# Kernel optimization log

Hardware: AMD Instinct MI355X
Metric: run time of the kernel (lower is better)

## Reference

```python
import jax, jax.numpy as jnp
import numpy as np

EPS_NORM = 1e-05
EPS_LOG = 1e-10


def _rmsnorm(x, scale, eps=EPS_NORM):
    var = jnp.mean(jnp.square(x), axis=-1, keepdims=True)
    return x * jax.lax.rsqrt(var + eps) * scale


def setup_inputs() -> dict:
    key = jax.random.key(0)
    k1, k2, k3, k4 = jax.random.split(key, 4)
    B, S, H, E, V = 1, 256, 2560, 10, 50257
    hidden_states = jax.random.normal(k1, (B, S, H), dtype=jnp.float32)
    embedding_matrix = jax.random.normal(k2, (V, H), dtype=jnp.float32) * 0.02
    norm_scale = jnp.ones((H,), dtype=jnp.float32)
    expert_weights = jax.random.normal(k3, (E, H, H), dtype=jnp.float32) * 0.02
    gate_weight = jax.random.normal(k4, (H, E), dtype=jnp.float32) * 0.02
    return {
        "hidden_states": hidden_states,
        "embedding_matrix": embedding_matrix,
        "norm_scale": norm_scale,
        "expert_weights": expert_weights,
        "gate_weight": gate_weight,
    }


def reference(hidden_states, embedding_matrix, norm_scale, expert_weights, gate_weight):
    # RMSNorm
    h = _rmsnorm(hidden_states, norm_scale)  # (B,S,H)
    # Per-expert dense transforms (no bias): (B,S,E,H)
    expert_hidden = jnp.einsum("bsh,ehd->bsed", h, expert_weights)
    # Shared-embedding projection: (B,S,E,V)
    expert_logits = jnp.einsum("bsed,vd->bsev", expert_hidden, embedding_matrix)
    # temperature == 1.0, no scaling
    expert_probs = jax.nn.softmax(expert_logits.astype(jnp.float32), axis=-1)
    # Gate over experts
    gate_logits = jnp.einsum("bsh,he->bse", h, gate_weight)
    gate_weights = jax.nn.softmax(gate_logits, axis=-1)  # (B,S,E)
    # Mixture of softmaxes, then log
    mixed_probs = jnp.einsum("bse,bsev->bsv", gate_weights, expert_probs)
    logits = jnp.log(mixed_probs + EPS_LOG)
    return logits
```

## Files before the change

### kernel.cpp

```cpp
#include <hip/hip_runtime.h>
#include <hip/hip_bf16.h>

#define SEQ   256
#define HDIM  2560
#define NEXP  10
#define VOC   50257
#define VP    50304
#define M2    2560
#define KTILES (HDIM/32)

#define O_H      0
#define O_EH     1310720
#define O_GATE   14417920
#define O_STATS  14428160
#define O_LOG    14448640
#define O_EMB    272005120
#define EMB_BYTES 257315840
#define WS_NEED  (O_EMB + (size_t)EMB_BYTES)

typedef __attribute__((ext_vector_type(8))) short bf16x8;
typedef __attribute__((ext_vector_type(4))) float f32x4;

union BPack { bf16x8 v; __hip_bfloat162 h[4]; };

__device__ __forceinline__ void ld_lds16(const void* g, void* l) {
  __builtin_amdgcn_global_load_lds(
      (const __attribute__((address_space(1))) void*)g,
      (__attribute__((address_space(3))) void*)l, 16, 0, 0);
}

__global__ __launch_bounds__(256) void cvt_emb_kernel(
    const float* __restrict__ src, __hip_bfloat16* __restrict__ dst) {
  const size_t n8 = (size_t)VOC * HDIM / 8;
  size_t i = (size_t)blockIdx.x * 256 + threadIdx.x;
  const size_t stride = (size_t)gridDim.x * 256;
  const f32x4* s4 = (const f32x4*)src;
  bf16x8* d8 = (bf16x8*)dst;
  for (; i < n8; i += stride) {
    const f32x4 x0 = s4[2 * i];
    const f32x4 x1 = s4[2 * i + 1];
    BPack u;
    u.h[0] = __float22bfloat162_rn(make_float2(x0.x, x0.y));
    u.h[1] = __float22bfloat162_rn(make_float2(x0.z, x0.w));
    u.h[2] = __float22bfloat162_rn(make_float2(x1.x, x1.y));
    u.h[3] = __float22bfloat162_rn(make_float2(x1.z, x1.w));
    d8[i] = u.v;
  }
}

__global__ __launch_bounds__(256) void rmsnorm_gate_kernel(
    const float* __restrict__ x, const float* __restrict__ scale,
    const float* __restrict__ gw, __hip_bfloat16* __restrict__ hbf,
    float* __restrict__ gate) {
  const int s   = blockIdx.x;
  const int tid = threadIdx.x;
  const int lane = tid & 63, wave = tid >> 6;
  const float* xr = x + (size_t)s * HDIM;

  float xi[10];
  float ss = 0.f;
#pragma unroll
  for (int j = 0; j < 10; ++j) {
    xi[j] = xr[j * 256 + tid];
    ss += xi[j] * xi[j];
  }
#pragma unroll
  for (int off = 32; off >= 1; off >>= 1) ss += __shfl_down(ss, off);
  __shared__ float red[4];
  if (lane == 0) red[wave] = ss;
  __syncthreads();
  const float tot = red[0] + red[1] + red[2] + red[3];
  const float inv = rsqrtf(tot / (float)HDIM + 1e-5f);

  float ge[NEXP];
#pragma unroll
  for (int e = 0; e < NEXP; ++e) ge[e] = 0.f;
#pragma unroll
  for (int j = 0; j < 10; ++j) {
    const int i = j * 256 + tid;
    const float hv = xi[j] * inv * scale[i];
    hbf[(size_t)s * HDIM + i] = __float2bfloat16(hv);
#pragma unroll
    for (int e = 0; e < NEXP; ++e) ge[e] += hv * gw[i * NEXP + e];
  }
#pragma unroll
  for (int e = 0; e < NEXP; ++e) {
#pragma unroll
    for (int off = 32; off >= 1; off >>= 1) ge[e] += __shfl_down(ge[e], off);
  }
  __shared__ float gred[4][NEXP];
  if (lane == 0) {
#pragma unroll
    for (int e = 0; e < NEXP; ++e) gred[wave][e] = ge[e];
  }
  __syncthreads();
  if (tid == 0) {
    float g[NEXP], mx = -1e30f, sum = 0.f;
#pragma unroll
    for (int e = 0; e < NEXP; ++e) {
      g[e] = gred[0][e] + gred[1][e] + gred[2][e] + gred[3][e];
      mx = fmaxf(mx, g[e]);
    }
#pragma unroll
    for (int e = 0; e < NEXP; ++e) { g[e] = __expf(g[e] - mx); sum += g[e]; }
#pragma unroll
    for (int e = 0; e < NEXP; ++e) gate[s * NEXP + e] = g[e] / sum;
  }
}

__global__ __launch_bounds__(256) void gemm1_kernel(
    const __hip_bfloat16* __restrict__ A, const float* __restrict__ W,
    __hip_bfloat16* __restrict__ EH) {
  __shared__ short As[128 * 32];
  __shared__ float Bs[32 * 128];

  const int tid = threadIdx.x;
  const int bm = blockIdx.x, bn = blockIdx.y, e = blockIdx.z;
  const int wave = tid >> 6, lane = tid & 63;
  const int wr = (wave & 1) * 64, wc = (wave >> 1) * 64;
  const int lm = lane & 15, lq = lane >> 4;
  const int row0 = bm * 128, col0 = bn * 128;
  const float* We = W + (size_t)e * HDIM * HDIM;

  f32x4 acc[4][4];
#pragma unroll
  for (int i = 0; i < 4; ++i)
#pragma unroll
    for (int j = 0; j < 4; ++j) acc[i][j] = (f32x4){0.f, 0.f, 0.f, 0.f};

  for (int kt = 0; kt < KTILES; ++kt) {
    const int k0 = kt * 32;
#pragma unroll
    for (int c = 0; c < 2; ++c) {
      const int ar = c * 64 + (tid >> 2);
      ld_lds16(A + (size_t)(row0 + ar) * HDIM + k0 + (tid & 3) * 8,
               (char*)As + c * 4096 + tid * 16);
    }
#pragma unroll
    for (int c = 0; c < 4; ++c) {
      const int L = c * 256 + tid;
      const int brow = L >> 5;
      const int cg = (L & 31) ^ (((brow >> 3) & 1) << 2);
      ld_lds16(We + (size_t)(k0 + brow) * HDIM + col0 + cg * 4,
               (char*)Bs + c * 4096 + tid * 16);
    }
    __syncthreads();

    bf16x8 a[4];
#pragma unroll
    for (int mt = 0; mt < 4; ++mt)
      a[mt] = *(const bf16x8*)&As[(wr + mt * 16 + lm) * 32 + lq * 8];
#pragma unroll
    for (int nt = 0; nt < 4; ++nt) {
      const int n = wc + nt * 16 + lm;
      const int slot = (n >> 2) ^ ((lq & 1) << 2);
      const int base = slot * 4 + (n & 3);
      BPack u;
#pragma unroll
      for (int jj = 0; jj < 4; ++jj) {
        const float f0 = Bs[(lq * 8 + 2 * jj) * 128 + base];
        const float f1 = Bs[(lq * 8 + 2 * jj + 1) * 128 + base];
        u.h[jj] = __float22bfloat162_rn(make_float2(f0, f1));
      }
#pragma unroll
      for (int mt = 0; mt < 4; ++mt)
        acc[mt][nt] = __builtin_amdgcn_mfma_f32_16x16x32_bf16(
            a[mt], u.v, acc[mt][nt], 0, 0, 0);
    }
    __syncthreads();
  }

#pragma unroll
  for (int mt = 0; mt < 4; ++mt) {
#pragma unroll
    for (int nt = 0; nt < 4; ++nt) {
#pragma unroll
      for (int i = 0; i < 4; ++i) {
        const int r = row0 + wr + mt * 16 + lq * 4 + i;
        const int d = col0 + wc + nt * 16 + lm;
        EH[((size_t)e * SEQ + r) * HDIM + d] = __float2bfloat16(acc[mt][nt][i]);
      }
    }
  }
}

__global__ __launch_bounds__(256) void gemm2_bf16_kernel(
    const __hip_bfloat16* __restrict__ A, const __hip_bfloat16* __restrict__ B,
    __hip_bfloat16* __restrict__ Cl) {
  __shared__ short As[128 * 32];
  __shared__ short Bs[128 * 32];

  const int tid = threadIdx.x;
  const int orig = blockIdx.x;
  const int q = 7860 / 8, rr = 7860 % 8;
  const int xcd = orig & 7, idx = orig >> 3;
  const int wg = (xcd < rr ? xcd * (q + 1) : rr * (q + 1) + (xcd - rr) * q) + idx;
  const int bm = wg % 20, bn = wg / 20;

  const int wave = tid >> 6, lane = tid & 63;
  const int wr = (wave & 1) * 64, wc = (wave >> 1) * 64;
  const int lm = lane & 15, lq = lane >> 4;
  const int row0 = bm * 128, col0 = bn * 128;

  f32x4 acc[4][4];
#pragma unroll
  for (int i = 0; i < 4; ++i)
#pragma unroll
    for (int j = 0; j < 4; ++j) acc[i][j] = (f32x4){0.f, 0.f, 0.f, 0.f};

  for (int kt = 0; kt < KTILES; ++kt) {
    const int k0 = kt * 32;
#pragma unroll
    for (int c = 0; c < 2; ++c) {
      const int ar = c * 64 + (tid >> 2);
      ld_lds16(A + (size_t)(row0 + ar) * HDIM + k0 + (tid & 3) * 8,
               (char*)As + c * 4096 + tid * 16);
    }
#pragma unroll
    for (int c = 0; c < 2; ++c) {
      const int br = c * 64 + (tid >> 2);
      const int vr = min(col0 + br, VOC - 1);
      ld_lds16(B + (size_t)vr * HDIM + k0 + (tid & 3) * 8,
               (char*)Bs + c * 4096 + tid * 16);
    }
    __syncthreads();

    bf16x8 a[4], b[4];
#pragma unroll
    for (int mt = 0; mt < 4; ++mt)
      a[mt] = *(const bf16x8*)&As[(wr + mt * 16 + lm) * 32 + lq * 8];
#pragma unroll
    for (int nt = 0; nt < 4; ++nt)
      b[nt] = *(const bf16x8*)&Bs[(wc + nt * 16 + lm) * 32 + lq * 8];
#pragma unroll
    for (int nt = 0; nt < 4; ++nt)
#pragma unroll
      for (int mt = 0; mt < 4; ++mt)
        acc[mt][nt] = __builtin_amdgcn_mfma_f32_16x16x32_bf16(
            a[mt], b[nt], acc[mt][nt], 0, 0, 0);
    __syncthreads();
  }

#pragma unroll
  for (int mt = 0; mt < 4; ++mt) {
#pragma unroll
    for (int nt = 0; nt < 4; ++nt) {
#pragma unroll
      for (int i = 0; i < 4; ++i) {
        const int r = row0 + wr + mt * 16 + lq * 4 + i;
        const int v = col0 + wc + nt * 16 + lm;
        const float val = (v < VOC) ? acc[mt][nt][i] : -INFINITY;
        Cl[(size_t)r * VP + v] = __float2bfloat16(val);
      }
    }
  }
}

__global__ __launch_bounds__(256) void gemm2_kernel(
    const __hip_bfloat16* __restrict__ A, const float* __restrict__ B,
    __hip_bfloat16* __restrict__ Cl) {
  __shared__ short As[128 * 32];
  __shared__ float Bs[128 * 32];

  const int tid = threadIdx.x;
  const int bm = blockIdx.x, bn = blockIdx.y;
  const int wave = tid >> 6, lane = tid & 63;
  const int wr = (wave & 1) * 64, wc = (wave >> 1) * 64;
  const int lm = lane & 15, lq = lane >> 4;
  const int row0 = bm * 128, col0 = bn * 128;

  f32x4 acc[4][4];
#pragma unroll
  for (int i = 0; i < 4; ++i)
#pragma unroll
    for (int j = 0; j < 4; ++j) acc[i][j] = (f32x4){0.f, 0.f, 0.f, 0.f};

  for (int kt = 0; kt < KTILES; ++kt) {
    const int k0 = kt * 32;
#pragma unroll
    for (int c = 0; c < 2; ++c) {
      const int ar = c * 64 + (tid >> 2);
      ld_lds16(A + (size_t)(row0 + ar) * HDIM + k0 + (tid & 3) * 8,
               (char*)As + c * 4096 + tid * 16);
    }
#pragma unroll
    for (int c = 0; c < 4; ++c) {
      const int L = c * 256 + tid;
      const int brow = L >> 3;
      const int cg = (L & 7) ^ (brow & 7);
      const int vr = min(col0 + brow, VOC - 1);
      ld_lds16(B + (size_t)vr * HDIM + k0 + cg * 4,
               (char*)Bs + c * 4096 + tid * 16);
    }
    __syncthreads();

    bf16x8 a[4];
#pragma unroll
    for (int mt = 0; mt < 4; ++mt)
      a[mt] = *(const bf16x8*)&As[(wr + mt * 16 + lm) * 32 + lq * 8];
#pragma unroll
    for (int nt = 0; nt < 4; ++nt) {
      const int n = wc + nt * 16 + lm;
      const int r7 = n & 7;
      const f32x4 b0 = *(const f32x4*)&Bs[n * 32 + (((2 * lq) ^ r7) << 2)];
      const f32x4 b1 = *(const f32x4*)&Bs[n * 32 + (((2 * lq + 1) ^ r7) << 2)];
      BPack u;
      u.h[0] = __float22bfloat162_rn(make_float2(b0.x, b0.y));
      u.h[1] = __float22bfloat162_rn(make_float2(b0.z, b0.w));
      u.h[2] = __float22bfloat162_rn(make_float2(b1.x, b1.y));
      u.h[3] = __float22bfloat162_rn(make_float2(b1.z, b1.w));
#pragma unroll
      for (int mt = 0; mt < 4; ++mt)
        acc[mt][nt] = __builtin_amdgcn_mfma_f32_16x16x32_bf16(
            a[mt], u.v, acc[mt][nt], 0, 0, 0);
    }
    __syncthreads();
  }

#pragma unroll
  for (int mt = 0; mt < 4; ++mt) {
#pragma unroll
    for (int nt = 0; nt < 4; ++nt) {
#pragma unroll
      for (int i = 0; i < 4; ++i) {
        const int r = row0 + wr + mt * 16 + lq * 4 + i;
        const int v = col0 + wc + nt * 16 + lm;
        const float val = (v < VOC) ? acc[mt][nt][i] : -INFINITY;
        Cl[(size_t)r * VP + v] = __float2bfloat16(val);
      }
    }
  }
}

__global__ __launch_bounds__(256) void softmax_stats_kernel(
    const __hip_bfloat16* __restrict__ Cl, const float* __restrict__ gate,
    float* __restrict__ stats) {
  const int r = blockIdx.x;
  const int tid = threadIdx.x;
  const bf16x8* row = (const bf16x8*)(Cl + (size_t)r * VP);

  float m = -1e30f, l = 0.f;
  for (int c = tid; c < VP / 8; c += 256) {
    const bf16x8 ch = row[c];
    float x[8];
#pragma unroll
    for (int j = 0; j < 8; ++j)
      x[j] = __bfloat162float(((const __hip_bfloat16*)&ch)[j]);
    float lm = x[0];
#pragma unroll
    for (int j = 1; j < 8; ++j) lm = fmaxf(lm, x[j]);
    if (lm > m) { l *= __expf(m - lm); m = lm; }
#pragma unroll
    for (int j = 0; j < 8; ++j) l += __expf(x[j] - m);
  }
#pragma unroll
  for (int off = 32; off >= 1; off >>= 1) {
    const float m2 = __shfl_down(m, off);
    const float l2 = __shfl_down(l, off);
    const float nm = fmaxf(m, m2);
    l = l * __expf(m - nm) + l2 * __expf(m2 - nm);
    m = nm;
  }
  __shared__ float sm[4], sl[4];
  if ((tid & 63) == 0) { sm[tid >> 6] = m; sl[tid >> 6] = l; }
  __syncthreads();
  if (tid == 0) {
    float M = sm[0], L = sl[0];
#pragma unroll
    for (int w = 1; w < 4; ++w) {
      const float nm = fmaxf(M, sm[w]);
      L = L * __expf(M - nm) + sl[w] * __expf(sm[w] - nm);
      M = nm;
    }
    const int e = r >> 8, s = r & 255;
    stats[2 * r] = M;
    stats[2 * r + 1] = gate[s * NEXP + e] / L;
  }
}

__global__ __launch_bounds__(256) void mix_kernel(
    const __hip_bfloat16* __restrict__ Cl, const float* __restrict__ stats,
    float* __restrict__ out) {
  const int s = blockIdx.y;
  const int v = blockIdx.x * 256 + threadIdx.x;
  if (v >= VOC) return;
  float acc = 1e-10f;
#pragma unroll
  for (int e = 0; e < NEXP; ++e) {
    const int r = e * SEQ + s;
    const float le = __bfloat162float(Cl[(size_t)r * VP + v]);
    acc = fmaf(stats[2 * r + 1], __expf(le - stats[2 * r]), acc);
  }
  out[(size_t)s * VOC + v] = __logf(acc);
}

extern "C" void kernel_launch(void* const* d_in, const int* in_sizes, int n_in,
                              void* d_out, int out_size, void* d_ws, size_t ws_size,
                              hipStream_t stream) {
  const float* x      = (const float*)d_in[0];
  const float* emb    = (const float*)d_in[1];
  const float* nscale = (const float*)d_in[2];
  const float* ew     = (const float*)d_in[3];
  const float* gw     = (const float*)d_in[4];
  float* out = (float*)d_out;

  char* ws = (char*)d_ws;
  __hip_bfloat16* hbf    = (__hip_bfloat16*)(ws + O_H);
  __hip_bfloat16* eh     = (__hip_bfloat16*)(ws + O_EH);
  float*          gate   = (float*)(ws + O_GATE);
  float*          stats  = (float*)(ws + O_STATS);
  __hip_bfloat16* logits = (__hip_bfloat16*)(ws + O_LOG);

  const bool have_emb_ws = (ws_size >= WS_NEED);

  if (have_emb_ws) {
    __hip_bfloat16* embb = (__hip_bfloat16*)(ws + O_EMB);
    cvt_emb_kernel<<<2048, 256, 0, stream>>>(emb, embb);
    rmsnorm_gate_kernel<<<SEQ, 256, 0, stream>>>(x, nscale, gw, hbf, gate);
    gemm1_kernel<<<dim3(2, HDIM / 128, NEXP), 256, 0, stream>>>(hbf, ew, eh);
    gemm2_bf16_kernel<<<(M2 / 128) * (VP / 128), 256, 0, stream>>>(eh, embb, logits);
  } else {
    rmsnorm_gate_kernel<<<SEQ, 256, 0, stream>>>(x, nscale, gw, hbf, gate);
    gemm1_kernel<<<dim3(2, HDIM / 128, NEXP), 256, 0, stream>>>(hbf, ew, eh);
    gemm2_kernel<<<dim3(M2 / 128, VP / 128), 256, 0, stream>>>(eh, emb, logits);
  }
  softmax_stats_kernel<<<M2, 256, 0, stream>>>(logits, gate, stats);
  mix_kernel<<<dim3((VOC + 255) / 256, SEQ), 256, 0, stream>>>(logits, stats, out);
}
```

Before: 1.843 ms.

## Replace bf16 logits GEMM with 256x256-tile, 512-thread, double-buffered pipelined kernel

Rewrites the main vocab-projection GEMM to use 256x256 output tiles with 8 waves, a 128KB LDS double buffer split into K-halves, and XOR-swizzled LDS layout. Global-to-LDS loads for the next tiles are issued between MFMA phases, with partial vmcnt waits and raised wave priority during MFMA bursts, so memory latency overlaps compute. The larger tile raises data reuse and arithmetic intensity, but it uses a large LDS footprint and many accumulator registers. It also adds boundary guards for the last N tile, which extends past the padded vocab width.

```diff
diff --git a/kernel.cpp b/kernel.cpp
--- a/kernel.cpp
+++ b/kernel.cpp
@@ -8,6 +8,7 @@
 #define VP    50304
 #define M2    2560
 #define KTILES (HDIM/32)
+#define NT2   (HDIM/64)
 
 #define O_H      0
 #define O_EH     1310720
@@ -184,73 +185,133 @@
   }
 }
 
-__global__ __launch_bounds__(256) void gemm2_bf16_kernel(
+__device__ __forceinline__ void stage_half(
+    const __hip_bfloat16* __restrict__ G, int rowbase, int kbase,
+    char* lds_half, int tid, bool clampB) {
+#pragma unroll
+  for (int c = 0; c < 2; ++c) {
+    const int line = c * 64 + (tid >> 3);
+    const int slog = (tid & 7) ^ (line & 7);
+    int row = rowbase + line + ((slog & 4) << 5);
+    if (clampB) row = min(row, VOC - 1);
+    ld_lds16(G + (size_t)row * HDIM + kbase + (slog & 3) * 8,
+             lds_half + c * 8192 + tid * 16);
+  }
+}
+
+__device__ __forceinline__ bf16x8 frag_rd(const char* half, int row, int lq) {
+  const int line = row & 127;
+  const int slot = (((row >> 7) << 2) | lq) ^ (line & 7);
+  return *(const bf16x8*)(half + line * 128 + slot * 16);
+}
+
+__device__ __forceinline__ void wait_barrier8() {
+  asm volatile("s_waitcnt vmcnt(8)" ::: "memory");
+  __builtin_amdgcn_s_barrier();
+  asm volatile("" ::: "memory");
+}
+
+__global__ __launch_bounds__(512) void gemm2_8ph_kernel(
     const __hip_bfloat16* __restrict__ A, const __hip_bfloat16* __restrict__ B,
     __hip_bfloat16* __restrict__ Cl) {
-  __shared__ short As[128 * 32];
-  __shared__ short Bs[128 * 32];
-
+  __shared__ char smem[131072];
   const int tid = threadIdx.x;
+  const int wave = tid >> 6, lane = tid & 63;
+  const int lm = lane & 15, lq = (lane >> 4) & 3;
+  const int wm = wave >> 2, wn = wave & 3;
+
   const int orig = blockIdx.x;
-  const int q = 7860 / 8, rr = 7860 % 8;
   const int xcd = orig & 7, idx = orig >> 3;
-  const int wg = (xcd < rr ? xcd * (q + 1) : rr * (q + 1) + (xcd - rr) * q) + idx;
-  const int bm = wg % 20, bn = wg / 20;
-
-  const int wave = tid >> 6, lane = tid & 63;
-  const int wr = (wave & 1) * 64, wc = (wave >> 1) * 64;
-  const int lm = lane & 15, lq = lane >> 4;
-  const int row0 = bm * 128, col0 = bn * 128;
-
-  f32x4 acc[4][4];
-#pragma unroll
-  for (int i = 0; i < 4; ++i)
+  const int wg = (xcd < 2 ? xcd * 247 : 494 + (xcd - 2) * 246) + idx;
+  const int bm = wg % 10, bn = wg / 10;
+  const int row0 = bm * 256, col0 = bn * 256;
+
+  f32x4 acc[8][4];
+#pragma unroll
+  for (int i = 0; i < 8; ++i)
 #pragma unroll
     for (int j = 0; j < 4; ++j) acc[i][j] = (f32x4){0.f, 0.f, 0.f, 0.f};
 
-  for (int kt = 0; kt < KTILES; ++kt) {
-    const int k0 = kt * 32;
-#pragma unroll
-    for (int c = 0; c < 2; ++c) {
-      const int ar = c * 64 + (tid >> 2);
-      ld_lds16(A + (size_t)(row0 + ar) * HDIM + k0 + (tid & 3) * 8,
-               (char*)As + c * 4096 + tid * 16);
-    }
-#pragma unroll
-    for (int c = 0; c < 2; ++c) {
-      const int br = c * 64 + (tid >> 2);
-      const int vr = min(col0 + br, VOC - 1);
-      ld_lds16(B + (size_t)vr * HDIM + k0 + (tid & 3) * 8,
-               (char*)Bs + c * 4096 + tid * 16);
-    }
-    __syncthreads();
-
-    bf16x8 a[4], b[4];
-#pragma unroll
-    for (int mt = 0; mt < 4; ++mt)
-      a[mt] = *(const bf16x8*)&As[(wr + mt * 16 + lm) * 32 + lq * 8];
-#pragma unroll
-    for (int nt = 0; nt < 4; ++nt)
-      b[nt] = *(const bf16x8*)&Bs[(wc + nt * 16 + lm) * 32 + lq * 8];
-#pragma unroll
-    for (int nt = 0; nt < 4; ++nt)
-#pragma unroll
-      for (int mt = 0; mt < 4; ++mt)
-        acc[mt][nt] = __builtin_amdgcn_mfma_f32_16x16x32_bf16(
-            a[mt], b[nt], acc[mt][nt], 0, 0, 0);
-    __syncthreads();
-  }
-
-#pragma unroll
-  for (int mt = 0; mt < 4; ++mt) {
+  stage_half(A, row0, 0,  smem + 0,     tid, false);
+  stage_half(B, col0, 0,  smem + 32768, tid, true);
+  stage_half(A, row0, 32, smem + 16384, tid, false);
+  stage_half(B, col0, 32, smem + 49152, tid, true);
+  stage_half(A, row0, 64, smem + 65536, tid, false);
+  stage_half(B, col0, 64, smem + 98304, tid, true);
+
+  const int arow = wm * 128 + lm;
+  const int brow = wn * 64 + lm;
+
+  for (int t = 0; t < NT2; ++t) {
+    char* rb = smem + (t & 1) * 65536;
+    char* wb = smem + ((t + 1) & 1) * 65536;
+    const char* A0 = rb;
+    const char* A1 = rb + 16384;
+    const char* B0 = rb + 32768;
+    const char* B1 = rb + 49152;
+
+    wait_barrier8();
+    bf16x8 a[8], b0, b1;
+#pragma unroll
+    for (int mt = 0; mt < 8; ++mt) a[mt] = frag_rd(A0, arow + mt * 16, lq);
+    b0 = frag_rd(B0, brow + 0, lq);
+    b1 = frag_rd(B0, brow + 16, lq);
+    if (t + 1 < NT2) stage_half(A, row0, (t + 1) * 64 + 32, wb + 16384, tid, false);
+    __builtin_amdgcn_s_setprio(1);
+#pragma unroll
+    for (int mt = 0; mt < 8; ++mt) {
+      acc[mt][0] = __builtin_amdgcn_mfma_f32_16x16x32_bf16(a[mt], b0, acc[mt][0], 0, 0, 0);
+      acc[mt][1] = __builtin_amdgcn_mfma_f32_16x16x32_bf16(a[mt], b1, acc[mt][1], 0, 0, 0);
+    }
+    __builtin_amdgcn_s_setprio(0);
+    b0 = frag_rd(B0, brow + 32, lq);
+    b1 = frag_rd(B0, brow + 48, lq);
+    if (t + 1 < NT2) stage_half(B, col0, (t + 1) * 64 + 32, wb + 49152, tid, true);
+    __builtin_amdgcn_s_setprio(1);
+#pragma unroll
+    for (int mt = 0; mt < 8; ++mt) {
+      acc[mt][2] = __builtin_amdgcn_mfma_f32_16x16x32_bf16(a[mt], b0, acc[mt][2], 0, 0, 0);
+      acc[mt][3] = __builtin_amdgcn_mfma_f32_16x16x32_bf16(a[mt], b1, acc[mt][3], 0, 0, 0);
+    }
+    __builtin_amdgcn_s_setprio(0);
+
+    wait_barrier8();
+#pragma unroll
+    for (int mt = 0; mt < 8; ++mt) a[mt] = frag_rd(A1, arow + mt * 16, lq);
+    b0 = frag_rd(B1, brow + 0, lq);
+    b1 = frag_rd(B1, brow + 16, lq);
+    if (t + 2 < NT2) stage_half(A, row0, (t + 2) * 64, rb, tid, false);
+    __builtin_amdgcn_s_setprio(1);
+#pragma unroll
+    for (int mt = 0; mt < 8; ++mt) {
+      acc[mt][0] = __builtin_amdgcn_mfma_f32_16x16x32_bf16(a[mt], b0, acc[mt][0], 0, 0, 0);
+      acc[mt][1] = __builtin_amdgcn_mfma_f32_16x16x32_bf16(a[mt], b1, acc[mt][1], 0, 0, 0);
+    }
+    __builtin_amdgcn_s_setprio(0);
+    b0 = frag_rd(B1, brow + 32, lq);
+    b1 = frag_rd(B1, brow + 48, lq);
+    if (t + 2 < NT2) stage_half(B, col0, (t + 2) * 64, rb + 32768, tid, true);
+    __builtin_amdgcn_s_setprio(1);
+#pragma unroll
+    for (int mt = 0; mt < 8; ++mt) {
+      acc[mt][2] = __builtin_amdgcn_mfma_f32_16x16x32_bf16(a[mt], b0, acc[mt][2], 0, 0, 0);
+      acc[mt][3] = __builtin_amdgcn_mfma_f32_16x16x32_bf16(a[mt], b1, acc[mt][3], 0, 0, 0);
+    }
+    __builtin_amdgcn_s_setprio(0);
+  }
+
+#pragma unroll
+  for (int mt = 0; mt < 8; ++mt) {
 #pragma unroll
     for (int nt = 0; nt < 4; ++nt) {
 #pragma unroll
       for (int i = 0; i < 4; ++i) {
-        const int r = row0 + wr + mt * 16 + lq * 4 + i;
-        const int v = col0 + wc + nt * 16 + lm;
-        const float val = (v < VOC) ? acc[mt][nt][i] : -INFINITY;
-        Cl[(size_t)r * VP + v] = __float2bfloat16(val);
+        const int r = row0 + wm * 128 + mt * 16 + lq * 4 + i;
+        const int v = col0 + wn * 64 + nt * 16 + lm;
+        if (v < VP) {
+          const float val = (v < VOC) ? acc[mt][nt][i] : -INFINITY;
+          Cl[(size_t)r * VP + v] = __float2bfloat16(val);
+        }
       }
     }
   }
@@ -418,7 +479,7 @@
     cvt_emb_kernel<<<2048, 256, 0, stream>>>(emb, embb);
     rmsnorm_gate_kernel<<<SEQ, 256, 0, stream>>>(x, nscale, gw, hbf, gate);
     gemm1_kernel<<<dim3(2, HDIM / 128, NEXP), 256, 0, stream>>>(hbf, ew, eh);
-    gemm2_bf16_kernel<<<(M2 / 128) * (VP / 128), 256, 0, stream>>>(eh, embb, logits);
+    gemm2_8ph_kernel<<<10 * 197, 512, 0, stream>>>(eh, embb, logits);
   } else {
     rmsnorm_gate_kernel<<<SEQ, 256, 0, stream>>>(x, nscale, gw, hbf, gate);
     gemm1_kernel<<<dim3(2, HDIM / 128, NEXP), 256, 0, stream>>>(hbf, ew, eh);
```

New measurement: 1.578 ms. 14.4% less time.
